# Optimization experiments

Hardware: AMD Instinct MI355X
Metric: run time of the kernel (lower is better)

Reference implementation:

```python
import jax, jax.numpy as jnp
import numpy as np

INPUT_SIZE = 1024
HIDDEN_SIZE = 1024
BATCH = 32768
LEARNING_RATE = 0.01
# First call: time_stamps is empty -> temporal_weight = 1.0
TEMPORAL_WEIGHT = 1.0


def setup_inputs() -> dict:
    key = jax.random.key(0)
    kx, kw = jax.random.split(key)
    x = jax.random.normal(kx, (BATCH, INPUT_SIZE), dtype=jnp.float32)
    # nn.Parameter(torch.randn(input_size, hidden_size) * 0.1)
    W = jax.random.normal(kw, (INPUT_SIZE, HIDDEN_SIZE), dtype=jnp.float32) * 0.1
    return {"x": x, "W": W}


def reference(x, W):
    # Forward: hidden = tanh(x @ W)
    hidden = jnp.tanh(x @ W)  # [B, H]
    # Hebbian update: sum_b lr * outer(x_b, hidden_b) * w(t) / B == lr * w(t)/B * x^T @ hidden
    batch = x.shape[0]
    delta_w = (LEARNING_RATE * TEMPORAL_WEIGHT / batch) * (x.T @ hidden)  # [I, H]
    new_W = jnp.clip(W + delta_w, -1.0, 1.0)
    return hidden, new_W
```

## Files before the change

kernel.cpp:

```cpp
#include <hip/hip_runtime.h>
#include <cstdint>

#define BB 32768
#define II 1024
#define HH 1024
#define SPLIT 16
#define KCH (BB/SPLIT)
#define NT1 (II/64)
#define NT2 (KCH/64)

typedef _Float16 f16;
typedef _Float16 f16x4 __attribute__((ext_vector_type(4)));
typedef _Float16 f16x8 __attribute__((ext_vector_type(8)));
typedef float f32x4 __attribute__((ext_vector_type(4)));

typedef const __attribute__((address_space(1))) void gvoid_t;
typedef __attribute__((address_space(3))) void lvoid_t;

__device__ __forceinline__ void gload16(const void* g, void* l){
    __builtin_amdgcn_global_load_lds((gvoid_t*)g, (lvoid_t*)l, 16, 0, 0);
}

__device__ __forceinline__ float tanh_fast(float s){
    float a = fabsf(s);
    float e = __expf(-2.0f * a);
    float t = __fdividef(1.0f - e, 1.0f + e);
    return s < 0.0f ? -t : t;
}

__global__ __launch_bounds__(256) void k_prep(const float* __restrict__ in,
                                              f16* __restrict__ cvt_out,
                                              f16* __restrict__ tr_out,
                                              int C, int R){
    __shared__ float lt[64*67];
    const int t = threadIdx.x;
    const int r0 = blockIdx.x*64, c0 = blockIdx.y*64;
    #pragma unroll
    for (int p=0; p<4; ++p){
        int r = p*16 + (t>>4);
        int c = (t&15)*4;
        float4 v = *(const float4*)&in[(size_t)(r0+r)*C + c0 + c];
        if (cvt_out){
            f16x4 hv = {(f16)v.x,(f16)v.y,(f16)v.z,(f16)v.w};
            *(f16x4*)&cvt_out[(size_t)(r0+r)*C + c0 + c] = hv;
        }
        lt[r*67 + c+0] = v.x;
        lt[r*67 + c+1] = v.y;
        lt[r*67 + c+2] = v.z;
        lt[r*67 + c+3] = v.w;
    }
    __syncthreads();
    const int c = t>>2, rb = (t&3)*16;
    f16x8 a, b;
    #pragma unroll
    for (int e=0; e<8; ++e) a[e] = (f16)lt[(rb+e)*67 + c];
    #pragma unroll
    for (int e=0; e<8; ++e) b[e] = (f16)lt[(rb+8+e)*67 + c];
    f16* o = &tr_out[(size_t)(c0+c)*R + r0 + rb];
    *(f16x8*)o = a;
    *(f16x8*)(o+8) = b;
}

template<bool MT>
__device__ __forceinline__ void stage_half(const f16* __restrict__ panel, int ld,
                                           int row0, int kcol0, char* lds_half,
                                           int wid, int lane){
    #pragma unroll
    for (int r=0;r<2;++r){
        int o = r*8192 + wid*1024 + lane*16;
        int rr = o>>7;
        int c0 = (o&127) ^ ((rr&7)<<4);
        if constexpr (!MT){
            const f16* src = panel + (size_t)(row0 + rr)*ld + kcol0 + (c0>>1);
            gload16(src, lds_half + r*8192 + wid*1024);
        } else {
            int h    = row0 + rr;
            int babs = kcol0 + (c0>>1);
            const f16* src = panel + (((size_t)(h>>4)*(BB>>4) + (babs>>4))<<8)
                                   + ((h&15)<<4) + (babs&8);
            gload16(src, lds_half + r*8192 + wid*1024);
        }
    }
}

#define RD_A(BUFA, mh) { \
    _Pragma("unroll") for (int m_=0;m_<4;++m_){ \
        af[m_][0] = *(const f16x8*)((BUFA) + rowA + (mh)*8192 + m_*2048 + ksw0); \
        af[m_][1] = *(const f16x8*)((BUFA) + rowA + (mh)*8192 + m_*2048 + ksw1); }}

#define RD_B(BUFB, nh) { \
    _Pragma("unroll") for (int n_=0;n_<2;++n_){ \
        bf[(nh)*2+n_][0] = *(const f16x8*)((BUFB) + rowB + (nh)*4096 + n_*2048 + ksw0); \
        bf[(nh)*2+n_][1] = *(const f16x8*)((BUFB) + rowB + (nh)*4096 + n_*2048 + ksw1); }}

#define MFMA_Q(mh,nh) { \
    __builtin_amdgcn_s_setprio(1); \
    _Pragma("unroll") for (int m_=0;m_<4;++m_){ \
      _Pragma("unroll") for (int n_=0;n_<2;++n_){ \
        _Pragma("unroll") for (int ks_=0;ks_<2;++ks_){ \
          acc[(mh)*4+m_][(nh)*2+n_] = __builtin_amdgcn_mfma_f32_16x16x32_f16( \
              af[m_][ks_], bf[(nh)*2+n_][ks_], acc[(mh)*4+m_][(nh)*2+n_], 0,0,0); }}} \
    __builtin_amdgcn_s_setprio(0); }

#define PH_SYNC1 { __builtin_amdgcn_s_barrier(); \
    asm volatile("s_waitcnt lgkmcnt(0)" ::: "memory"); \
    __builtin_amdgcn_sched_barrier(0); }
#define PH_SYNC2 { __builtin_amdgcn_s_barrier(); }

template<bool BMT>
__device__ __forceinline__ void kloop8(const f16* __restrict__ Ap, int lda, int arow0,
                                       const f16* __restrict__ Bp, int ldb, int brow0,
                                       int kbase, int nt, char* sm,
                                       f32x4 (&acc)[8][4])
{
    const int t = threadIdx.x, lane = t & 63, wid = t >> 6;
    const int wr = wid >> 2, wc = wid & 3;
    const int fr = lane & 15, kg = lane >> 4;
    const int mask = nt - 1;
    char* const A0 = sm;
    char* const B0 = sm + 32768;
    char* const A1 = sm + 65536;
    char* const B1 = sm + 98304;
    const int rowA = wr*16384 + fr*128;
    const int rowB = (wc>>1)*16384 + (wc&1)*8192 + fr*128;
    const int ksw0 = ((kg    ) ^ (fr & 7)) << 4;
    const int ksw1 = ((kg + 4) ^ (fr & 7)) << 4;

    f16x8 af[4][2], bf[4][2];

    stage_half<false>(Ap, lda, arow0 +   0, kbase +  0, A0,         wid, lane);
    stage_half<false>(Ap, lda, arow0 + 128, kbase +  0, A0 + 16384, wid, lane);
    stage_half<BMT  >(Bp, ldb, brow0 +   0, kbase +  0, B0,         wid, lane);
    stage_half<BMT  >(Bp, ldb, brow0 + 128, kbase +  0, B0 + 16384, wid, lane);
    stage_half<BMT  >(Bp, ldb, brow0 +   0, kbase + 64, B1,         wid, lane);
    stage_half<false>(Ap, lda, arow0 +   0, kbase + 64, A1,         wid, lane);
    asm volatile("s_waitcnt vmcnt(4)" ::: "memory");
    __builtin_amdgcn_s_barrier();

    const int ni = nt >> 1;
    for (int it = 0; it < ni; ++it){
        const int k1 = (2*it + 1) * 64;
        const int k2 = ((2*it + 2) & mask) * 64;
        const int k3 = ((2*it + 3) & mask) * 64;
        RD_A(A0, 0); RD_B(B0, 0);
        stage_half<false>(Ap, lda, arow0 + 128, kbase + k1, A1 + 16384, wid, lane);
        PH_SYNC1; MFMA_Q(0,0); PH_SYNC2;
        RD_B(B0, 1);
        stage_half<BMT>(Bp, ldb, brow0 + 128, kbase + k1, B1 + 16384, wid, lane);
        PH_SYNC1; MFMA_Q(0,1); PH_SYNC2;
        RD_A(A0, 1);
        stage_half<BMT>(Bp, ldb, brow0 +   0, kbase + k2, B0, wid, lane);
        PH_SYNC1; MFMA_Q(1,0); PH_SYNC2;
        stage_half<false>(Ap, lda, arow0 +   0, kbase + k2, A0, wid, lane);
        PH_SYNC1; MFMA_Q(1,1);
        asm volatile("s_waitcnt vmcnt(4)" ::: "memory");
        __builtin_amdgcn_s_barrier();
        RD_A(A1, 0); RD_B(B1, 0);
        stage_half<false>(Ap, lda, arow0 + 128, kbase + k2, A0 + 16384, wid, lane);
        PH_SYNC1; MFMA_Q(0,0); PH_SYNC2;
        RD_B(B1, 1);
        stage_half<BMT>(Bp, ldb, brow0 + 128, kbase + k2, B0 + 16384, wid, lane);
        PH_SYNC1; MFMA_Q(0,1); PH_SYNC2;
        RD_A(A1, 1);
        stage_half<BMT>(Bp, ldb, brow0 +   0, kbase + k3, B1, wid, lane);
        PH_SYNC1; MFMA_Q(1,0); PH_SYNC2;
        stage_half<false>(Ap, lda, arow0 +   0, kbase + k3, A1, wid, lane);
        PH_SYNC1; MFMA_Q(1,1);
        asm volatile("s_waitcnt vmcnt(4)" ::: "memory");
        __builtin_amdgcn_s_barrier();
    }
    asm volatile("s_waitcnt vmcnt(0)" ::: "memory");
    __builtin_amdgcn_s_barrier();
}

__global__ __launch_bounds__(512,2) void k_gemm1(const f16* __restrict__ xf,
                                                 const f16* __restrict__ wt,
                                                 float* __restrict__ hidden,
                                                 f16* __restrict__ ht){
    __shared__ char sm[131072];
    const int bid = (int)blockIdx.x;
    const int swz = (bid & 7)*64 + (bid >> 3);
    const int btile = swz >> 2, htile = swz & 3;
    f32x4 acc[8][4] = {};
    kloop8<false>(xf, II, btile*256, wt, II, htile*256, 0, NT1, sm, acc);

    const int t = threadIdx.x, lane = t & 63, wid = t >> 6;
    const int wr = wid >> 2, wc = wid & 3;
    const int fr = lane & 15, kg = lane >> 4;
    const int b_base = btile*256 + wr*128 + kg*4;
    const int h_base = htile*256 + wc*64 + fr;
    #pragma unroll
    for (int mf=0; mf<8; ++mf){
        const int b = b_base + mf*16;
        #pragma unroll
        for (int nf=0; nf<4; ++nf){
            const int h = h_base + nf*16;
            float t0 = tanh_fast(acc[mf][nf][0]);
            float t1 = tanh_fast(acc[mf][nf][1]);
            float t2 = tanh_fast(acc[mf][nf][2]);
            float t3 = tanh_fast(acc[mf][nf][3]);
            f16x4 hv = {(f16)t0,(f16)t1,(f16)t2,(f16)t3};
            *(f16x4*)&ht[(((size_t)(h>>4)*(BB>>4) + (b>>4))<<8) + ((h&15)<<4) + (b&15)] = hv;
            hidden[(size_t)(b+0)*HH + h] = t0;
            hidden[(size_t)(b+1)*HH + h] = t1;
            hidden[(size_t)(b+2)*HH + h] = t2;
            hidden[(size_t)(b+3)*HH + h] = t3;
        }
    }
}

__global__ __launch_bounds__(512,2) void k_gemm2(const f16* __restrict__ xt,
                                                 const f16* __restrict__ ht,
                                                 f16* __restrict__ part){
    __shared__ char sm[131072];
    const int bid = (int)blockIdx.x;
    const int swz = (bid & 7)*32 + (bid >> 3);
    const int split = swz >> 4, tile = swz & 15;
    const int itile = tile & 3, htile = tile >> 2;
    f32x4 acc[8][4] = {};
    kloop8<true>(xt, BB, itile*256, ht, BB, htile*256, split*KCH, NT2, sm, acc);

    const int t = threadIdx.x, lane = t & 63, wid = t >> 6;
    const int wr = wid >> 2, wc = wid & 3;
    const int fr = lane & 15, kg = lane >> 4;
    const size_t pb = (size_t)split*II*HH;
    #pragma unroll
    for (int mf=0; mf<8; ++mf){
        const int i0 = itile*256 + wr*128 + mf*16 + kg*4;
        #pragma unroll
        for (int nf=0; nf<4; ++nf){
            const int h = htile*256 + wc*64 + nf*16 + fr;
            f16x4 pv = {(f16)acc[mf][nf][0],(f16)acc[mf][nf][1],
                        (f16)acc[mf][nf][2],(f16)acc[mf][nf][3]};
            *(f16x4*)&part[pb + (((size_t)(i0>>4)*(HH>>4) + (h>>4))<<8) + ((h&15)<<4) + (i0&15)] = pv;
        }
    }
}

__global__ __launch_bounds__(256) void k_final(const f16* __restrict__ part,
                                               const float* __restrict__ W,
                                               float* __restrict__ outW){
    const int T = (int)blockIdx.x*256 + threadIdx.x;
    const int mt = T >> 5;
    const int hl = (T & 31) >> 1;
    const int ihalf = T & 1;
    const int i0 = (mt >> 6)*16 + ihalf*8;
    const int h  = (mt & 63)*16 + hl;
    const size_t po = ((size_t)mt << 8) + (hl << 4) + ihalf*8;
    float s[8] = {};
    #pragma unroll
    for (int sp=0; sp<SPLIT; ++sp){
        f16x8 p = *(const f16x8*)&part[(size_t)sp*1048576 + po];
        #pragma unroll
        for (int e=0;e<8;++e) s[e] += (float)p[e];
    }
    const float SCALE = 3.0517578125e-07f;
    #pragma unroll
    for (int e=0;e<8;++e){
        const size_t o = (size_t)(i0+e)*HH + h;
        outW[o] = fminf(1.f, fmaxf(-1.f, fmaf(SCALE, s[e], W[o])));
    }
}

extern "C" void kernel_launch(void* const* d_in, const int* in_sizes, int n_in,
                              void* d_out, int out_size, void* d_ws, size_t ws_size,
                              hipStream_t stream){
    (void)in_sizes; (void)n_in; (void)out_size; (void)ws_size;
    const float* x = (const float*)d_in[0];
    const float* W = (const float*)d_in[1];
    float* hidden = (float*)d_out;
    float* outW   = hidden + (size_t)BB*HH;
    char* ws = (char*)d_ws;
    f16* xf   = (f16*)(ws);
    f16* xt   = (f16*)(ws + 67108864ull);
    f16* ht   = (f16*)(ws + 134217728ull);
    f16* wt   = (f16*)(ws + 201326592ull);
    f16* part = (f16*)(ws);

    k_prep<<<dim3(BB/64, II/64), 256, 0, stream>>>(x, xf, xt, II, BB);
    k_prep<<<dim3(II/64, HH/64), 256, 0, stream>>>(W, nullptr, wt, HH, II);
    k_gemm1<<<dim3((BB/256)*(HH/256)), 512, 0, stream>>>(xf, wt, hidden, ht);
    k_gemm2<<<dim3(16*SPLIT), 512, 0, stream>>>(xt, ht, part);
    k_final<<<dim3((II*HH)/(256*8)), 256, 0, stream>>>(part, W, outW);
}
```

Before: 233.7 us.

## Merge prep launches, add nontemporal loads/stores, relax LDS wait before first MFMA

Fuses the two prep kernels (x and W conversion/transposition) into one launch by choosing the source from the block index, which saves one kernel launch and its tail. Marks streaming global loads and stores (x reads, hidden writes, partial reads, outW writes) as nontemporal to reduce cache pollution. Inserts an lgkmcnt(8) wait before the first MFMA phase sync of each half-iteration in the GEMM loop. The nontemporal hints may change L2 behaviour, and the extra wait adds only a partial LDS wait ahead of the existing full lgkmcnt(0) in PH_SYNC1.

```diff
diff --git a/kernel.cpp b/kernel.cpp
--- a/kernel.cpp
+++ b/kernel.cpp
@@ -28,26 +28,31 @@
     return s < 0.0f ? -t : t;
 }
 
-__global__ __launch_bounds__(256) void k_prep(const float* __restrict__ in,
-                                              f16* __restrict__ cvt_out,
-                                              f16* __restrict__ tr_out,
-                                              int C, int R){
+__global__ __launch_bounds__(256) void k_prep2(const float* __restrict__ x,
+                                               f16* __restrict__ xf,
+                                               f16* __restrict__ xt,
+                                               const float* __restrict__ W,
+                                               f16* __restrict__ wt){
     __shared__ float lt[64*67];
     const int t = threadIdx.x;
-    const int r0 = blockIdx.x*64, c0 = blockIdx.y*64;
+    const int bx = (int)blockIdx.x;
+    const float* in; f16* cvt; f16* tr; int C, R, r0;
+    if (bx < 512){ in = x; cvt = xf; tr = xt; C = II; R = BB; r0 = bx*64; }
+    else         { in = W; cvt = nullptr; tr = wt; C = HH; R = II; r0 = (bx-512)*64; }
+    const int c0 = blockIdx.y*64;
     #pragma unroll
     for (int p=0; p<4; ++p){
         int r = p*16 + (t>>4);
         int c = (t&15)*4;
-        float4 v = *(const float4*)&in[(size_t)(r0+r)*C + c0 + c];
-        if (cvt_out){
-            f16x4 hv = {(f16)v.x,(f16)v.y,(f16)v.z,(f16)v.w};
-            *(f16x4*)&cvt_out[(size_t)(r0+r)*C + c0 + c] = hv;
-        }
-        lt[r*67 + c+0] = v.x;
-        lt[r*67 + c+1] = v.y;
-        lt[r*67 + c+2] = v.z;
-        lt[r*67 + c+3] = v.w;
+        f32x4 v = __builtin_nontemporal_load((const f32x4*)&in[(size_t)(r0+r)*C + c0 + c]);
+        if (cvt){
+            f16x4 hv = {(f16)v[0],(f16)v[1],(f16)v[2],(f16)v[3]};
+            *(f16x4*)&cvt[(size_t)(r0+r)*C + c0 + c] = hv;
+        }
+        lt[r*67 + c+0] = v[0];
+        lt[r*67 + c+1] = v[1];
+        lt[r*67 + c+2] = v[2];
+        lt[r*67 + c+3] = v[3];
     }
     __syncthreads();
     const int c = t>>2, rb = (t&3)*16;
@@ -56,7 +61,7 @@
     for (int e=0; e<8; ++e) a[e] = (f16)lt[(rb+e)*67 + c];
     #pragma unroll
     for (int e=0; e<8; ++e) b[e] = (f16)lt[(rb+8+e)*67 + c];
-    f16* o = &tr_out[(size_t)(c0+c)*R + r0 + rb];
+    f16* o = &tr[(size_t)(c0+c)*R + r0 + rb];
     *(f16x8*)o = a;
     *(f16x8*)(o+8) = b;
 }
@@ -106,6 +111,7 @@
     asm volatile("s_waitcnt lgkmcnt(0)" ::: "memory"); \
     __builtin_amdgcn_sched_barrier(0); }
 #define PH_SYNC2 { __builtin_amdgcn_s_barrier(); }
+#define LGKM8 { asm volatile("s_waitcnt lgkmcnt(8)" ::: "memory"); }
 
 template<bool BMT>
 __device__ __forceinline__ void kloop8(const f16* __restrict__ Ap, int lda, int arow0,
@@ -144,7 +150,7 @@
         const int k3 = ((2*it + 3) & mask) * 64;
         RD_A(A0, 0); RD_B(B0, 0);
         stage_half<false>(Ap, lda, arow0 + 128, kbase + k1, A1 + 16384, wid, lane);
-        PH_SYNC1; MFMA_Q(0,0); PH_SYNC2;
+        LGKM8; PH_SYNC1; MFMA_Q(0,0); PH_SYNC2;
         RD_B(B0, 1);
         stage_half<BMT>(Bp, ldb, brow0 + 128, kbase + k1, B1 + 16384, wid, lane);
         PH_SYNC1; MFMA_Q(0,1); PH_SYNC2;
@@ -157,7 +163,7 @@
         __builtin_amdgcn_s_barrier();
         RD_A(A1, 0); RD_B(B1, 0);
         stage_half<false>(Ap, lda, arow0 + 128, kbase + k2, A0 + 16384, wid, lane);
-        PH_SYNC1; MFMA_Q(0,0); PH_SYNC2;
+        LGKM8; PH_SYNC1; MFMA_Q(0,0); PH_SYNC2;
         RD_B(B1, 1);
         stage_half<BMT>(Bp, ldb, brow0 + 128, kbase + k2, B0 + 16384, wid, lane);
         PH_SYNC1; MFMA_Q(0,1); PH_SYNC2;
@@ -201,10 +207,10 @@
             float t3 = tanh_fast(acc[mf][nf][3]);
             f16x4 hv = {(f16)t0,(f16)t1,(f16)t2,(f16)t3};
             *(f16x4*)&ht[(((size_t)(h>>4)*(BB>>4) + (b>>4))<<8) + ((h&15)<<4) + (b&15)] = hv;
-            hidden[(size_t)(b+0)*HH + h] = t0;
-            hidden[(size_t)(b+1)*HH + h] = t1;
-            hidden[(size_t)(b+2)*HH + h] = t2;
-            hidden[(size_t)(b+3)*HH + h] = t3;
+            __builtin_nontemporal_store(t0, &hidden[(size_t)(b+0)*HH + h]);
+            __builtin_nontemporal_store(t1, &hidden[(size_t)(b+1)*HH + h]);
+            __builtin_nontemporal_store(t2, &hidden[(size_t)(b+2)*HH + h]);
+            __builtin_nontemporal_store(t3, &hidden[(size_t)(b+3)*HH + h]);
         }
     }
 }
@@ -250,7 +256,7 @@
     float s[8] = {};
     #pragma unroll
     for (int sp=0; sp<SPLIT; ++sp){
-        f16x8 p = *(const f16x8*)&part[(size_t)sp*1048576 + po];
+        f16x8 p = __builtin_nontemporal_load((const f16x8*)&part[(size_t)sp*1048576 + po]);
         #pragma unroll
         for (int e=0;e<8;++e) s[e] += (float)p[e];
     }
@@ -258,7 +264,8 @@
     #pragma unroll
     for (int e=0;e<8;++e){
         const size_t o = (size_t)(i0+e)*HH + h;
-        outW[o] = fminf(1.f, fmaxf(-1.f, fmaf(SCALE, s[e], W[o])));
+        float r = fminf(1.f, fmaxf(-1.f, fmaf(SCALE, s[e], W[o])));
+        __builtin_nontemporal_store(r, &outW[o]);
     }
 }
 
@@ -277,8 +284,7 @@
     f16* wt   = (f16*)(ws + 201326592ull);
     f16* part = (f16*)(ws);
 
-    k_prep<<<dim3(BB/64, II/64), 256, 0, stream>>>(x, xf, xt, II, BB);
-    k_prep<<<dim3(II/64, HH/64), 256, 0, stream>>>(W, nullptr, wt, HH, II);
+    k_prep2<<<dim3(528, 16), 256, 0, stream>>>(x, xf, xt, W, wt);
     k_gemm1<<<dim3((BB/256)*(HH/256)), 512, 0, stream>>>(xf, wt, hidden, ht);
     k_gemm2<<<dim3(16*SPLIT), 512, 0, stream>>>(xt, ht, part);
     k_final<<<dim3((II*HH)/(256*8)), 256, 0, stream>>>(part, W, outW);
```

Result: faster. 212.0 us (-9.3%).
